# Kernel tuning notes

Hardware: AMD Instinct MI355X
Metric: run time of the kernel (lower is better)

The kernel has to match this reference:

```python
import jax, jax.numpy as jnp
import numpy as np

B, N, D_IN, D_PROJ, C = 1024, 50000, 768, 128, 100
BW2 = float(D_PROJ)   # RBF bandwidth^2
EPS = 1e-10


def setup_inputs() -> dict:
    key = jax.random.key(0)
    ks = jax.random.split(key, 6)
    x = jax.random.normal(ks[0], (B, D_IN), jnp.float32)
    X = jax.random.normal(ks[1], (N, D_IN), jnp.float32)
    # learned projection (Linear D_IN -> D_PROJ); scale keeps projected coords ~N(0,1)
    Wp = jax.random.normal(ks[2], (D_IN, D_PROJ), jnp.float32) * (D_IN ** -0.5)
    bp = jnp.zeros((D_PROJ,), jnp.float32)
    Y = jax.random.randint(ks[3], (N,), 0, C, jnp.int32)
    SorP_train = jax.random.normal(ks[4], (N, C), jnp.float32)
    SorP_q = jax.random.normal(ks[5], (B, C), jnp.float32)
    return dict(x=x, X=X, Wp=Wp, bp=bp, Y=Y, SorP_train=SorP_train, SorP_q=SorP_q)


def _perm_locs(SorP):
    # locs = argsort(argsort(SorP, descending)) per row
    sort_idx = jnp.argsort(-SorP, axis=-1)
    return jnp.argsort(sort_idx, axis=-1)


def reference(x, X, Wp, bp, Y, SorP_train, SorP_q):
    px = x @ Wp + bp            # [B, D_PROJ]
    pX = X @ Wp + bp            # [N, D_PROJ]
    # squared euclidean distances via GEMM
    sqd = ((px * px).sum(-1, keepdims=True)
           + (pX * pX).sum(-1)[None, :]
           - 2.0 * (px @ pX.T))                     # [B, N]
    Kis = jnp.exp(-sqd / (2.0 * BW2))               # RBF kernel, self-sim == 1
    # drop_self: zero out (near-)self matches
    Kis = jnp.where(Kis < 1.0 - EPS, Kis, 0.0)
    # rows with ~zero total mass -> uniform eps
    Kis = jnp.where(Kis.sum(1, keepdims=True) > EPS, Kis, EPS)
    # MODE_SORT label encoding: one_hot(locs_train[i, Y[i]])
    locs_t = _perm_locs(SorP_train)                 # [N, C]
    Y1h = jax.nn.one_hot(locs_t[jnp.arange(N), Y], C, dtype=jnp.float32)
    pred = Kis @ Y1h                                # [B, C]
    pred = pred / pred.sum(1, keepdims=True)
    # per-sample reorder (vectorized gather instead of the python loop)
    locs_q = _perm_locs(SorP_q)                     # [B, C]
    return jnp.take_along_axis(pred, locs_q, axis=1)
```

## Files before the change

### kernel.cpp

```cpp
#include <hip/hip_runtime.h>


typedef short  bf8v  __attribute__((ext_vector_type(8)));
typedef float  f32x4 __attribute__((ext_vector_type(4)));

#define NTRAIN 50000
#define NPAD   50048
#define NTILES 391
#define BQ     1024
#define DIN    768
#define DP     128
#define NCLS   100
#define PSTRIDE 102
#define PCOLS  104
#define FIXS   2097152.0f
#define FIXI   (1.0f / 2097152.0f)
#define NBX    (NPAD / 64)
#define NBQ    (BQ / 64)
#define NBL    ((NPAD + 3) / 4)

__device__ __forceinline__ short f2bf(float x) {
    unsigned u = __float_as_uint(x);
    u += 0x7FFFu + ((u >> 16) & 1u);
    return (short)(u >> 16);
}
__device__ __forceinline__ float bf2f(unsigned short u) {
    return __uint_as_float((unsigned)u << 16);
}

#define AS1U(p) ((const __attribute__((address_space(1))) unsigned int*)(unsigned long long)(p))
#define AS3U(p) ((__attribute__((address_space(3))) unsigned int*)(unsigned int)(unsigned long long)(p))

__global__ __launch_bounds__(256) void k_pack_wp(const float* __restrict__ Wp,
                                                 short* __restrict__ WpP) {
    int tid = blockIdx.x * 256 + threadIdx.x;
    if (tid >= 24 * 8 * 64) return;
    int l = tid & 63, cb = (tid >> 6) & 7, q = tid >> 9;
    int c = cb * 16 + (l & 15);
    int g = l >> 4;
    bf8v o;
#pragma unroll
    for (int j = 0; j < 8; ++j) {
        int k = q * 32 + g * 8 + j;
        o[j] = f2bf(Wp[k * DP + c]);
    }
    *reinterpret_cast<bf8v*>(WpP + (size_t)tid * 8) = o;
}

__device__ __forceinline__ void proj_body(const float* __restrict__ Xin,
                                          const short* __restrict__ WpP,
                                          const float* __restrict__ bp,
                                          short* __restrict__ outP,
                                          float* __restrict__ normv,
                                          int Mreal, int blk,
                                          float* __restrict__ Xlds) {
    const int tid = threadIdx.x;
    const int w = tid >> 6, l = tid & 63, g = l >> 4, li = l & 15;
    const int rowblk = blk * 64;

    f32x4 acc[8];
#pragma unroll
    for (int cb = 0; cb < 8; ++cb) acc[cb] = (f32x4){0.f, 0.f, 0.f, 0.f};

#define STAGE64(lbuf, kb)                                                     \
    {                                                                         \
        _Pragma("unroll")                                                     \
        for (int it = 0; it < 4; ++it) {                                      \
            int s  = w * 256 + it * 64 + l;                                   \
            int r  = s >> 4;                                                  \
            int c4 = (s & 15) ^ (r & 7);                                      \
            int rg = rowblk + r;                                              \
            rg = (rg < Mreal) ? rg : (Mreal - 1);                             \
            const float* gp = Xin + (size_t)rg * DIN + (kb) * 64 + c4 * 4;    \
            const float* lp = (lbuf) + (w * 256 + it * 64) * 4;               \
            __builtin_amdgcn_global_load_lds(AS1U(gp), AS3U(lp), 16, 0, 0);   \
        }                                                                     \
    }
#define ISSUE_B(dst, kb)                                                      \
    {                                                                         \
        _Pragma("unroll")                                                     \
        for (int f = 0; f < 16; ++f)                                          \
            dst[f] = *reinterpret_cast<const bf8v*>(                          \
                WpP + ((size_t)((kb) * 16 + f) * 64 + l) * 8);                \
    }

    bf8v breg[16];
    float4 a[4];

    STAGE64(Xlds, 0);
    STAGE64(Xlds + 4096, 1);
    ISSUE_B(breg, 0);

#pragma unroll 1
    for (int kb = 0; kb < 12; ++kb) {
        float* tb = Xlds + (kb & 1) * 4096;
        asm volatile("s_waitcnt vmcnt(20)" ::: "memory");
        {
            const float* rbase = tb + (w * 16 + li) * 64;
#pragma unroll
            for (int kc = 0; kc < 2; ++kc) {
                int s0 = (kc * 8 + g * 2)     ^ (li & 7);
                int s1 = (kc * 8 + g * 2 + 1) ^ (li & 7);
                a[kc * 2]     = *reinterpret_cast<const float4*>(rbase + s0 * 4);
                a[kc * 2 + 1] = *reinterpret_cast<const float4*>(rbase + s1 * 4);
            }
        }
        asm volatile("s_waitcnt lgkmcnt(0)" ::: "memory");
        __builtin_amdgcn_sched_barrier(0);
        if (kb + 2 < 12) {
            STAGE64(tb, kb + 2);
            asm volatile("s_waitcnt vmcnt(4)" ::: "memory");
        } else {
            asm volatile("s_waitcnt vmcnt(0)" ::: "memory");
        }
        __builtin_amdgcn_sched_barrier(0);
#pragma unroll
        for (int kc = 0; kc < 2; ++kc) {
            float4 a0 = a[kc * 2], a1 = a[kc * 2 + 1];
            bf8v af;
            af[0] = f2bf(a0.x); af[1] = f2bf(a0.y);
            af[2] = f2bf(a0.z); af[3] = f2bf(a0.w);
            af[4] = f2bf(a1.x); af[5] = f2bf(a1.y);
            af[6] = f2bf(a1.z); af[7] = f2bf(a1.w);
#pragma unroll
            for (int cb = 0; cb < 8; ++cb)
                acc[cb] = __builtin_amdgcn_mfma_f32_16x16x32_bf16(
                              af, breg[kc * 8 + cb], acc[cb], 0, 0, 0);
        }
        if (kb + 1 < 12) ISSUE_B(breg, kb + 1);
    }
#undef STAGE64
#undef ISSUE_B

    float bpv[8];
#pragma unroll
    for (int cb = 0; cb < 8; ++cb) bpv[cb] = bp[cb * 16 + li];
#pragma unroll
    for (int cb = 0; cb < 8; ++cb)
#pragma unroll
        for (int r = 0; r < 4; ++r) acc[cb][r] += bpv[cb];

#pragma unroll
    for (int r = 0; r < 4; ++r) {
        float s = 0.f;
#pragma unroll
        for (int cb = 0; cb < 8; ++cb) {
            float v = acc[cb][r];
            s += v * v;
        }
        s += __shfl_xor(s, 1);
        s += __shfl_xor(s, 2);
        s += __shfl_xor(s, 4);
        s += __shfl_xor(s, 8);
        int grow = rowblk + w * 16 + 4 * g + r;
        if (li == 0) normv[grow] = (grow < Mreal) ? s : 1e30f;
    }

#pragma unroll
    for (int cb = 0; cb < 8; ++cb) {
        int d = cb * 16 + li;
        int q = d >> 5, g2 = (d & 31) >> 3, j = d & 7;
#pragma unroll
        for (int r = 0; r < 4; ++r) {
            int grow = rowblk + w * 16 + 4 * g + r;
            float v = (grow < Mreal) ? acc[cb][r] : 0.f;
            size_t e = ((size_t)((grow >> 4) * 4 + q) * 64 +
                        (g2 * 16 + (grow & 15))) * 8 + j;
            outP[e] = f2bf(v);
        }
    }
}

__global__ __launch_bounds__(256, 3) void k_front(const float* __restrict__ X,
                                                  const float* __restrict__ x,
                                                  const short* __restrict__ WpP,
                                                  const float* __restrict__ bp,
                                                  short* __restrict__ pXp,
                                                  short* __restrict__ pxq,
                                                  float* __restrict__ kn,
                                                  float* __restrict__ qn,
                                                  const float* __restrict__ S,
                                                  const int* __restrict__ Y,
                                                  int* __restrict__ lab) {
    __shared__ __align__(16) float Xlds[2 * 64 * 64];
    int b = blockIdx.x;
    if (b < NBX) {
        proj_body(X, WpP, bp, pXp, kn, NTRAIN, b, Xlds);
        return;
    }
    if (b < NBX + NBQ) {
        proj_body(x, WpP, bp, pxq, qn, BQ, b - NBX, Xlds);
        return;
    }
    int w = threadIdx.x >> 6, l = threadIdx.x & 63;
    int i = (b - NBX - NBQ) * 4 + w;
    if (i >= NPAD) return;
    int cnt = 0;
    if (i < NTRAIN) {
        int y = Y[i];
        float t = S[(size_t)i * NCLS + y];
        float v1 = S[(size_t)i * NCLS + l];
        bool p1 = (v1 > t) || (v1 == t && l < y);
        unsigned long long b1 = __ballot(p1);
        bool p2 = false;
        if (l < NCLS - 64) {
            float v2 = S[(size_t)i * NCLS + 64 + l];
            p2 = (v2 > t) || (v2 == t && (64 + l) < y);
        }
        unsigned long long b2 = __ballot(p2);
        cnt = __popcll(b1) + __popcll(b2);
    }
    if (l == 0) lab[i] = cnt;
}

__global__ __launch_bounds__(256) void k_main(const short* __restrict__ pxp,
                                              const short* __restrict__ pXp,
                                              const float* __restrict__ qn,
                                              const float* __restrict__ kn,
                                              const int* __restrict__ lab,
                                              unsigned short* __restrict__ part,
                                              int NCH) {
    __shared__ __align__(16) unsigned plds[128 * PSTRIDE];
    const int tid = threadIdx.x;
    const int w = tid >> 6, l = tid & 63, g = l >> 4, li = l & 15;
    const int ch = blockIdx.x;
    const int bt = blockIdx.y;

    for (int s = tid; s < 128 * PSTRIDE; s += 256) plds[s] = 0u;
    __syncthreads();

    bf8v af[2][4];
#pragma unroll
    for (int rb = 0; rb < 2; ++rb)
#pragma unroll
        for (int q = 0; q < 4; ++q) {
            int RB = bt * 8 + w * 2 + rb;
            af[rb][q] = *reinterpret_cast<const bf8v*>(
                            pxp + (size_t)((RB * 4 + q) * 64 + l) * 8);
        }
    float qnv[2][4];
#pragma unroll
    for (int rb = 0; rb < 2; ++rb)
#pragma unroll
        for (int r = 0; r < 4; ++r)
            qnv[rb][r] = qn[bt * 128 + w * 32 + rb * 16 + 4 * g + r];

#pragma unroll 1
    for (int t = ch; t < NTILES; t += NCH) {
        const int i0 = t * 128;
        const int RB0 = i0 >> 4;
        float knv8[8];
        int   labv8[8];
#pragma unroll
        for (int ib = 0; ib < 8; ++ib) {
            knv8[ib]  = kn[i0 + ib * 16 + li];
            labv8[ib] = lab[i0 + ib * 16 + li];
        }
        bf8v bfr[4][4];
#pragma unroll
        for (int p = 0; p < 3; ++p)
#pragma unroll
            for (int q = 0; q < 4; ++q)
                bfr[p][q] = *reinterpret_cast<const bf8v*>(
                    pXp + (size_t)(((RB0 + p) * 4 + q) * 64 + l) * 8);
#pragma unroll
        for (int ib = 0; ib < 8; ++ib) {
            if (ib + 3 < 8) {
#pragma unroll
                for (int q = 0; q < 4; ++q)
                    bfr[(ib + 3) & 3][q] = *reinterpret_cast<const bf8v*>(
                        pXp + (size_t)(((RB0 + ib + 3) * 4 + q) * 64 + l) * 8);
            }
            f32x4 s0 = (f32x4){0.f, 0.f, 0.f, 0.f};
            f32x4 s1 = (f32x4){0.f, 0.f, 0.f, 0.f};
#pragma unroll
            for (int q = 0; q < 4; ++q) {
                s0 = __builtin_amdgcn_mfma_f32_16x16x32_bf16(af[0][q], bfr[ib & 3][q], s0, 0, 0, 0);
                s1 = __builtin_amdgcn_mfma_f32_16x16x32_bf16(af[1][q], bfr[ib & 3][q], s1, 0, 0, 0);
            }
            const float knv  = knv8[ib];
            const int   labv = labv8[ib];
#pragma unroll
            for (int rb = 0; rb < 2; ++rb) {
                f32x4 sv = rb ? s1 : s0;
#pragma unroll
                for (int r = 0; r < 4; ++r) {
                    float sqd = qnv[rb][r] + knv - 2.f * sv[r];
                    float kis = __expf(sqd * (-1.f / 256.f));
                    kis = (kis < 1.0f) ? kis : 0.f;
                    unsigned qv = (unsigned)__float2uint_rn(kis * FIXS);
                    int rowl = w * 32 + rb * 16 + 4 * g + r;
                    atomicAdd(&plds[rowl * PSTRIDE + labv], qv);
                }
            }
        }
    }

#pragma unroll 1
    for (int rr = 0; rr < 32; ++rr) {
        int row = w * 32 + rr;
        if (l < PSTRIDE / 2) {
            uint2 u = *reinterpret_cast<const uint2*>(&plds[row * PSTRIDE + l * 2]);
            float vx = (float)u.x * FIXI, vy = (float)u.y * FIXI;
            unsigned pk = (unsigned)(unsigned short)f2bf(vx) |
                          ((unsigned)(unsigned short)f2bf(vy) << 16);
            int grow = bt * 128 + row;
            *reinterpret_cast<unsigned*>(
                &part[((size_t)grow * NCH + ch) * PCOLS + l * 2]) = pk;
        }
    }
}

__global__ __launch_bounds__(256) void k_final(const unsigned short* __restrict__ part,
                                               const float* __restrict__ SorPq,
                                               float* __restrict__ out,
                                               int NCH) {
    __shared__ float sp[NCLS];
    __shared__ float pr2[2][PCOLS];
    int t = threadIdx.x, b = blockIdx.x;
    int c = t & 127, h = t >> 7;
    if (h == 1 && c < NCLS) sp[c] = SorPq[(size_t)b * NCLS + c];
    if (c < NCLS) {
        float s = 0.f;
        int half = NCH >> 1;
        const unsigned short* p =
            part + ((size_t)b * NCH + (size_t)h * half) * PCOLS + c;
        for (int ch = 0; ch < half; ++ch) s += bf2f(p[(size_t)ch * PCOLS]);
        pr2[h][c] = s;
    }
    __syncthreads();
    if (t < NCLS) pr2[0][t] += pr2[1][t];
    __syncthreads();
    if (t < NCLS) {
        float tot = 0.f;
        for (int k = 0; k < NCLS; ++k) tot += pr2[0][k];
        float s = sp[t];
        int r = 0;
        for (int k = 0; k < NCLS; ++k) {
            float sk = sp[k];
            r += (sk > s || (sk == s && k < t)) ? 1 : 0;
        }
        out[(size_t)b * NCLS + t] = pr2[0][r] / tot;
    }
}

extern "C" void kernel_launch(void* const* d_in, const int* in_sizes, int n_in,
                              void* d_out, int out_size, void* d_ws, size_t ws_size,
                              hipStream_t stream) {
    const float* x    = (const float*)d_in[0];
    const float* X    = (const float*)d_in[1];
    const float* Wp   = (const float*)d_in[2];
    const float* bp   = (const float*)d_in[3];
    const int*   Y    = (const int*)  d_in[4];
    const float* SPt  = (const float*)d_in[5];
    const float* SPq  = (const float*)d_in[6];
    float* out = (float*)d_out;

    char* ws = (char*)d_ws;
    short* WpP = (short*)(ws + 0);
    short* pXp = (short*)(ws + 196608);
    short* pxq = (short*)(ws + 13008896);
    float* kn  = (float*)(ws + 13271040);
    float* qn  = (float*)(ws + 13471232);
    int*   lab = (int*)  (ws + 13475328);
    unsigned short* part = (unsigned short*)(ws + 13675520);

    const size_t base = 13675520;
    const size_t per  = (size_t)BQ * PCOLS * 2;
    int NCH = 96;
    if (ws_size > base) {
        size_t fit = (ws_size - base) / per;
        if ((size_t)NCH > fit) NCH = (int)fit;
    } else {
        NCH = 8;
    }
    NCH &= ~7;
    if (NCH < 8) NCH = 8;

    k_pack_wp<<<48, 256, 0, stream>>>(Wp, WpP);
    k_front<<<NBX + NBQ + NBL, 256, 0, stream>>>(X, x, WpP, bp, pXp, pxq,
                                                 kn, qn, SPt, Y, lab);
    k_main<<<dim3(NCH, 8), 256, 0, stream>>>(pxq, pXp, qn, kn, lab, part, NCH);
    k_final<<<BQ, 256, 0, stream>>>(part, SPq, out, NCH);
}
```

Measured before the change: 111.3 us.

## Use 2-wave blocks with 32 rows per wave in projection front kernel

```diff
diff --git a/kernel.cpp b/kernel.cpp
--- a/kernel.cpp
+++ b/kernel.cpp
@@ -57,22 +57,25 @@
     const int tid = threadIdx.x;
     const int w = tid >> 6, l = tid & 63, g = l >> 4, li = l & 15;
     const int rowblk = blk * 64;
-
-    f32x4 acc[8];
-#pragma unroll
-    for (int cb = 0; cb < 8; ++cb) acc[cb] = (f32x4){0.f, 0.f, 0.f, 0.f};
-
-#define STAGE64(lbuf, kb)                                                     \
+    float* wbase = Xlds + w * 4096;
+
+    f32x4 acc[2][8];
+#pragma unroll
+    for (int rb = 0; rb < 2; ++rb)
+#pragma unroll
+        for (int cb = 0; cb < 8; ++cb) acc[rb][cb] = (f32x4){0.f, 0.f, 0.f, 0.f};
+
+#define STAGE32(buf, kb)                                                      \
     {                                                                         \
         _Pragma("unroll")                                                     \
-        for (int it = 0; it < 4; ++it) {                                      \
-            int s  = w * 256 + it * 64 + l;                                   \
-            int r  = s >> 4;                                                  \
-            int c4 = (s & 15) ^ (r & 7);                                      \
-            int rg = rowblk + r;                                              \
+        for (int it = 0; it < 8; ++it) {                                      \
+            int sl   = it * 64 + l;                                           \
+            int rloc = sl >> 4;                                               \
+            int c4   = (sl & 15) ^ (rloc & 7);                                \
+            int rg   = rowblk + w * 32 + rloc;                                \
             rg = (rg < Mreal) ? rg : (Mreal - 1);                             \
             const float* gp = Xin + (size_t)rg * DIN + (kb) * 64 + c4 * 4;    \
-            const float* lp = (lbuf) + (w * 256 + it * 64) * 4;               \
+            const float* lp = (buf) + it * 256;                               \
             __builtin_amdgcn_global_load_lds(AS1U(gp), AS3U(lp), 16, 0, 0);   \
         }                                                                     \
     }
@@ -85,93 +88,102 @@
     }
 
     bf8v breg[16];
-    float4 a[4];
-
-    STAGE64(Xlds, 0);
-    STAGE64(Xlds + 4096, 1);
+    float4 a8[8];
+
+    STAGE32(wbase, 0);
+    STAGE32(wbase + 2048, 1);
     ISSUE_B(breg, 0);
 
 #pragma unroll 1
     for (int kb = 0; kb < 12; ++kb) {
-        float* tb = Xlds + (kb & 1) * 4096;
-        asm volatile("s_waitcnt vmcnt(20)" ::: "memory");
-        {
-            const float* rbase = tb + (w * 16 + li) * 64;
-#pragma unroll
-            for (int kc = 0; kc < 2; ++kc) {
+        float* tb = wbase + (kb & 1) * 2048;
+        asm volatile("s_waitcnt vmcnt(24)" ::: "memory");
+#pragma unroll
+        for (int kc = 0; kc < 2; ++kc)
+#pragma unroll
+            for (int rb = 0; rb < 2; ++rb) {
+                int rloc = rb * 16 + li;
+                const float* rbase = tb + rloc * 64;
                 int s0 = (kc * 8 + g * 2)     ^ (li & 7);
                 int s1 = (kc * 8 + g * 2 + 1) ^ (li & 7);
-                a[kc * 2]     = *reinterpret_cast<const float4*>(rbase + s0 * 4);
-                a[kc * 2 + 1] = *reinterpret_cast<const float4*>(rbase + s1 * 4);
-            }
-        }
+                a8[kc * 4 + rb * 2]     = *reinterpret_cast<const float4*>(rbase + s0 * 4);
+                a8[kc * 4 + rb * 2 + 1] = *reinterpret_cast<const float4*>(rbase + s1 * 4);
+            }
         asm volatile("s_waitcnt lgkmcnt(0)" ::: "memory");
         __builtin_amdgcn_sched_barrier(0);
         if (kb + 2 < 12) {
-            STAGE64(tb, kb + 2);
-            asm volatile("s_waitcnt vmcnt(4)" ::: "memory");
+            STAGE32(tb, kb + 2);
+            asm volatile("s_waitcnt vmcnt(8)" ::: "memory");
         } else {
             asm volatile("s_waitcnt vmcnt(0)" ::: "memory");
         }
         __builtin_amdgcn_sched_barrier(0);
 #pragma unroll
-        for (int kc = 0; kc < 2; ++kc) {
-            float4 a0 = a[kc * 2], a1 = a[kc * 2 + 1];
-            bf8v af;
-            af[0] = f2bf(a0.x); af[1] = f2bf(a0.y);
-            af[2] = f2bf(a0.z); af[3] = f2bf(a0.w);
-            af[4] = f2bf(a1.x); af[5] = f2bf(a1.y);
-            af[6] = f2bf(a1.z); af[7] = f2bf(a1.w);
-#pragma unroll
-            for (int cb = 0; cb < 8; ++cb)
-                acc[cb] = __builtin_amdgcn_mfma_f32_16x16x32_bf16(
-                              af, breg[kc * 8 + cb], acc[cb], 0, 0, 0);
-        }
+        for (int kc = 0; kc < 2; ++kc)
+#pragma unroll
+            for (int rb = 0; rb < 2; ++rb) {
+                float4 a0 = a8[kc * 4 + rb * 2], a1 = a8[kc * 4 + rb * 2 + 1];
+                bf8v af;
+                af[0] = f2bf(a0.x); af[1] = f2bf(a0.y);
+                af[2] = f2bf(a0.z); af[3] = f2bf(a0.w);
+                af[4] = f2bf(a1.x); af[5] = f2bf(a1.y);
+                af[6] = f2bf(a1.z); af[7] = f2bf(a1.w);
+#pragma unroll
+                for (int cb = 0; cb < 8; ++cb)
+                    acc[rb][cb] = __builtin_amdgcn_mfma_f32_16x16x32_bf16(
+                                      af, breg[kc * 8 + cb], acc[rb][cb], 0, 0, 0);
+            }
         if (kb + 1 < 12) ISSUE_B(breg, kb + 1);
     }
-#undef STAGE64
+#undef STAGE32
 #undef ISSUE_B
 
     float bpv[8];
 #pragma unroll
     for (int cb = 0; cb < 8; ++cb) bpv[cb] = bp[cb * 16 + li];
 #pragma unroll
-    for (int cb = 0; cb < 8; ++cb)
-#pragma unroll
-        for (int r = 0; r < 4; ++r) acc[cb][r] += bpv[cb];
-
-#pragma unroll
-    for (int r = 0; r < 4; ++r) {
-        float s = 0.f;
+    for (int rb = 0; rb < 2; ++rb)
+#pragma unroll
+        for (int cb = 0; cb < 8; ++cb)
+#pragma unroll
+            for (int r = 0; r < 4; ++r) acc[rb][cb][r] += bpv[cb];
+
+#pragma unroll
+    for (int rb = 0; rb < 2; ++rb)
+#pragma unroll
+        for (int r = 0; r < 4; ++r) {
+            float s = 0.f;
+#pragma unroll
+            for (int cb = 0; cb < 8; ++cb) {
+                float v = acc[rb][cb][r];
+                s += v * v;
+            }
+            s += __shfl_xor(s, 1);
+            s += __shfl_xor(s, 2);
+            s += __shfl_xor(s, 4);
+            s += __shfl_xor(s, 8);
+            int grow = rowblk + w * 32 + rb * 16 + 4 * g + r;
+            if (li == 0) normv[grow] = (grow < Mreal) ? s : 1e30f;
+        }
+
+#pragma unroll
+    for (int rb = 0; rb < 2; ++rb)
 #pragma unroll
         for (int cb = 0; cb < 8; ++cb) {
-            float v = acc[cb][r];
-            s += v * v;
-        }
-        s += __shfl_xor(s, 1);
-        s += __shfl_xor(s, 2);
-        s += __shfl_xor(s, 4);
-        s += __shfl_xor(s, 8);
-        int grow = rowblk + w * 16 + 4 * g + r;
-        if (li == 0) normv[grow] = (grow < Mreal) ? s : 1e30f;
-    }
-
-#pragma unroll
-    for (int cb = 0; cb < 8; ++cb) {
-        int d = cb * 16 + li;
-        int q = d >> 5, g2 = (d & 31) >> 3, j = d & 7;
-#pragma unroll
-        for (int r = 0; r < 4; ++r) {
-            int grow = rowblk + w * 16 + 4 * g + r;
-            float v = (grow < Mreal) ? acc[cb][r] : 0.f;
-            size_t e = ((size_t)((grow >> 4) * 4 + q) * 64 +
-                        (g2 * 16 + (grow & 15))) * 8 + j;
-            outP[e] = f2bf(v);
-        }
-    }
-}
-
-__global__ __launch_bounds__(256, 3) void k_front(const float* __restrict__ X,
+            int d = cb * 16 + li;
+            int q = d >> 5, g2 = (d & 31) >> 3, j = d & 7;
+#pragma unroll
+            for (int r = 0; r < 4; ++r) {
+                int grow = rowblk + w * 32 + rb * 16 + 4 * g + r;
+                float v = (grow < Mreal) ? acc[rb][cb][r] : 0.f;
+                size_t e = ((size_t)((grow >> 4) * 4 + q) * 64 +
+                            (g2 * 16 + (grow & 15))) * 8 + j;
+                outP[e] = f2bf(v);
+            }
+        }
+}
+
+__global__ __launch_bounds__(128, 2) void k_front(const float* __restrict__ X,
                                                   const float* __restrict__ x,
                                                   const short* __restrict__ WpP,
                                                   const float* __restrict__ bp,
@@ -182,7 +194,7 @@
                                                   const float* __restrict__ S,
                                                   const int* __restrict__ Y,
                                                   int* __restrict__ lab) {
-    __shared__ __align__(16) float Xlds[2 * 64 * 64];
+    __shared__ __align__(16) float Xlds[2 * 2 * 2048];
     int b = blockIdx.x;
     if (b < NBX) {
         proj_body(X, WpP, bp, pXp, kn, NTRAIN, b, Xlds);
@@ -193,24 +205,27 @@
         return;
     }
     int w = threadIdx.x >> 6, l = threadIdx.x & 63;
-    int i = (b - NBX - NBQ) * 4 + w;
-    if (i >= NPAD) return;
-    int cnt = 0;
-    if (i < NTRAIN) {
-        int y = Y[i];
-        float t = S[(size_t)i * NCLS + y];
-        float v1 = S[(size_t)i * NCLS + l];
-        bool p1 = (v1 > t) || (v1 == t && l < y);
-        unsigned long long b1 = __ballot(p1);
-        bool p2 = false;
-        if (l < NCLS - 64) {
-            float v2 = S[(size_t)i * NCLS + 64 + l];
-            p2 = (v2 > t) || (v2 == t && (64 + l) < y);
-        }
-        unsigned long long b2 = __ballot(p2);
-        cnt = __popcll(b1) + __popcll(b2);
-    }
-    if (l == 0) lab[i] = cnt;
+#pragma unroll
+    for (int r2 = 0; r2 < 2; ++r2) {
+        int i = (b - NBX - NBQ) * 4 + w * 2 + r2;
+        if (i >= NPAD) continue;
+        int cnt = 0;
+        if (i < NTRAIN) {
+            int y = Y[i];
+            float t = S[(size_t)i * NCLS + y];
+            float v1 = S[(size_t)i * NCLS + l];
+            bool p1 = (v1 > t) || (v1 == t && l < y);
+            unsigned long long b1 = __ballot(p1);
+            bool p2 = false;
+            if (l < NCLS - 64) {
+                float v2 = S[(size_t)i * NCLS + 64 + l];
+                p2 = (v2 > t) || (v2 == t && (64 + l) < y);
+            }
+            unsigned long long b2 = __ballot(p2);
+            cnt = __popcll(b1) + __popcll(b2);
+        }
+        if (l == 0) lab[i] = cnt;
+    }
 }
 
 __global__ __launch_bounds__(256) void k_main(const short* __restrict__ pxp,
@@ -378,7 +393,7 @@
     if (NCH < 8) NCH = 8;
 
     k_pack_wp<<<48, 256, 0, stream>>>(Wp, WpP);
-    k_front<<<NBX + NBQ + NBL, 256, 0, stream>>>(X, x, WpP, bp, pXp, pxq,
+    k_front<<<NBX + NBQ + NBL, 128, 0, stream>>>(X, x, WpP, bp, pXp, pxq,
                                                  kn, qn, SPt, Y, lab);
     k_main<<<dim3(NCH, 8), 256, 0, stream>>>(pxq, pXp, qn, kn, lab, part, NCH);
     k_final<<<BQ, 256, 0, stream>>>(part, SPq, out, NCH);
```

Measured after the change: 111.9 us. Within noise of the previous version (+0.6%).
